# Kernel tuning notes

Hardware: AMD Instinct MI355X
Metric: run time of the kernel (lower is better)

## Reference

```python
import jax, jax.numpy as jnp
from jax import lax
import numpy as np

P = 128      # stored adversarial patch resolution
WIN = 256    # max pasted-patch extent (>= max patch_size = sqrt(300*300*0.4) ~ 190)
MINH = 60.0  # min_patch_height
H, W, B, N = 896, 896, 8, 24


def _bilinear(img, ys, xs):
    """Bilinearly sample img [h,w,c] on the grid ys x xs -> [len(ys), len(xs), c]."""
    h, w = img.shape[0], img.shape[1]
    ys = jnp.clip(ys, 0.0, h - 1.0)
    xs = jnp.clip(xs, 0.0, w - 1.0)
    y0 = jnp.floor(ys); x0 = jnp.floor(xs)
    y0i = y0.astype(jnp.int32); x0i = x0.astype(jnp.int32)
    y1i = jnp.minimum(y0i + 1, h - 1); x1i = jnp.minimum(x0i + 1, w - 1)
    wy = (ys - y0)[:, None, None]; wx = (xs - x0)[None, :, None]
    v00 = img[y0i][:, x0i]; v01 = img[y0i][:, x1i]
    v10 = img[y1i][:, x0i]; v11 = img[y1i][:, x1i]
    return (1 - wy) * ((1 - wx) * v00 + wx * v01) + wy * ((1 - wx) * v10 + wx * v11)


def setup_inputs() -> dict:
    key = jax.random.key(0)
    ks = jax.random.split(key, 8)
    ymin = jax.random.uniform(ks[0], (B, N), minval=0.0, maxval=H - 320.0)
    bh = jax.random.uniform(ks[1], (B, N), minval=80.0, maxval=300.0)
    xmin = jax.random.uniform(ks[2], (B, N), minval=0.0, maxval=W - 320.0)
    bw = jax.random.uniform(ks[3], (B, N), minval=80.0, maxval=300.0)
    boxes = jnp.stack([ymin, xmin, ymin + bh, xmin + bw], axis=-1)
    images = jax.random.uniform(ks[4], (B, H, W, 3))
    patch = jax.random.uniform(ks[5], (P, P, 3))
    Ws = jax.random.normal(ks[6], (2, 1)) * 0.5
    bs = jnp.zeros((1,), jnp.float32)
    Wg = jax.random.normal(ks[7], (2, P * P)) * 0.5
    bg = jnp.zeros((P * P,), jnp.float32)
    return {"boxes": boxes, "images": images, "patch": patch,
            "Ws": Ws, "bs": bs, "Wg": Wg, "bg": bg}


def reference(boxes, images, patch, Ws, bs, Wg, bg):
    Bx, Hx, Wx, C = images.shape
    Hf, Wf = float(Hx), float(Wx)
    mu_p = patch.mean((0, 1)); sd_p = patch.std((0, 1)) + 1e-6

    def per_image(image, bxs):
        bh = (bxs[:, 2] - bxs[:, 0]) / Hf
        bw = (bxs[:, 3] - bxs[:, 1]) / Wf
        feats = jnp.stack([bh, bw], axis=-1)                      # [N,2]
        scales = jax.nn.sigmoid(feats @ Ws + bs)[:, 0] * 0.4
        # Patcher.create (vectorized over boxes)
        h = bxs[:, 2] - bxs[:, 0]; w = bxs[:, 3] - bxs[:, 1]
        ps = jnp.floor(jnp.sqrt(h * w * scales))                  # square patch side
        oy = bxs[:, 0] + h / 2.0; ox = bxs[:, 1] + w / 2.0
        ymp = jnp.maximum(oy - ps / 2.0, 0.0)
        xmp = jnp.maximum(ox - ps / 2.0, 0.0)
        ymp = jnp.where(ymp + ps > Hf, Hf - ps, ymp)
        xmp = jnp.where(xmp + ps > Wf, Wf - ps, xmp)
        pboxes = jnp.stack([ymp, xmp, ps, ps], axis=-1)           # [N,4]
        valid = ps > MINH                                          # filter-by-mask
        masks = jax.nn.sigmoid(feats @ Wg + bg).reshape(-1, P, P, 1)  # gen masks
        img_p = jnp.pad(image, ((0, WIN), (0, WIN), (0, 0)))

        def body(carry, inp):
            imgc, bgl = carry
            pbox, mask, vld = inp
            yi = pbox[0].astype(jnp.int32); xi = pbox[1].astype(jnp.int32)
            ph = pbox[2].astype(jnp.int32); pw = pbox[3].astype(jnp.int32)
            phf = jnp.maximum(ph, 1).astype(jnp.float32)
            pwf = jnp.maximum(pw, 1).astype(jnp.float32)
            # crop background region -> fixed PxP
            ys = yi.astype(jnp.float32) + (jnp.arange(P, dtype=jnp.float32) + 0.5) * phf / P - 0.5
            xs = xi.astype(jnp.float32) + (jnp.arange(P, dtype=jnp.float32) + 0.5) * pwf / P - 0.5
            patch_bg = _bilinear(imgc, ys, xs)                    # [P,P,C]
            # histogram (moment) matching of patch to local background
            mu_b = patch_bg.mean((0, 1)); sd_b = patch_bg.std((0, 1)) + 1e-6
            matched = (patch - mu_p) / sd_p * sd_b + mu_b
            blended = jnp.where(mask > 0.5, matched, patch_bg)
            r = jnp.arange(WIN, dtype=jnp.float32)
            sy = (r + 0.5) * P / phf - 0.5
            sx = (r + 0.5) * P / pwf - 0.5
            im_win = _bilinear(blended, sy, sx)
            win = lax.dynamic_slice(imgc, (yi, xi, 0), (WIN, WIN, imgc.shape[-1]))
            inside = (jnp.arange(WIN)[:, None] < ph) & (jnp.arange(WIN)[None, :] < pw) & vld
            upd = jnp.where(inside[..., None], im_win, win)
            imgc = lax.dynamic_update_slice(imgc, upd, (yi, xi, 0))
            bgl = bgl + jnp.where(vld, mask.mean(), 0.0)          # generator.bg_loss
            return (imgc, bgl), None

        (img_p, bgl), _ = lax.scan(body, (img_p, jnp.zeros((), jnp.float32)),
                                   (pboxes, masks, valid))
        # scale loss over valid boxes: mean + 0.5*variance
        vf = valid.astype(jnp.float32)
        n = jnp.maximum(vf.sum(), 1.0)
        m = (scales * vf).sum() / n
        var = (vf * (scales - m) ** 2).sum() / n
        return img_p[:Hx, :Wx], bgl + m + 0.5 * var

    out, losses = jax.vmap(per_image)(images, boxes)
    return out, losses.sum()
```

## Files before the change

kernel.cpp:

```cpp
#include <hip/hip_runtime.h>

#define PPX  128
#define PP2  16384
#define IMH  896
#define IMW  896
#define NB   24
#define NI   8
#define HP   1152
#define WP   1152
#define MAXG 6
#define NMB  (NI*NB*8)
#define NCPY 2048
#define M1   12

#define WS_BOX  8
#define WS_MASK 2048
#define WS_SCH  100352
#define WS_LIST 100608
#define WS_MSUM 101760
#define WS_PART 103424
#define WS_PBG  140288

__device__ __forceinline__ void box_geom(const float* __restrict__ bx,
    const float* __restrict__ Wsc, const float* __restrict__ bsc,
    float& scale, float& ps, int& yi, int& xi, int& ph, int& vld)
{
  float ya=bx[0], xa=bx[1], yb=bx[2], xb=bx[3];
  float bh=(yb-ya)/(float)IMH, bw=(xb-xa)/(float)IMW;
  float z = bh*Wsc[0]+bw*Wsc[1]+bsc[0];
  float sig = 1.f/(1.f+expf(-z));
  scale = sig*0.4f;
  float h=yb-ya, w=xb-xa;
  ps = floorf(sqrtf((h*w)*scale));
  float oy=ya+h*0.5f, ox=xa+w*0.5f;
  float ymp=fmaxf(oy-ps*0.5f,0.f), xmp=fmaxf(ox-ps*0.5f,0.f);
  if (ymp+ps>(float)IMH) ymp=(float)IMH-ps;
  if (xmp+ps>(float)IMW) xmp=(float)IMW-ps;
  yi=(int)ymp; xi=(int)xmp; ph=(int)ps;
  vld = (ps>60.f) ? 1 : 0;
}

__device__ __forceinline__ void analytic3(int rr, int cc, float phf,
    const float* __restrict__ pbg1, const float* __restrict__ patch,
    const unsigned* msk, const float* ab, float v[3])
{
  float sy = ((rr + 0.5f)*128.0f)/phf - 0.5f;
  float sx = ((cc + 0.5f)*128.0f)/phf - 0.5f;
  sy = fminf(fmaxf(sy, 0.f), 127.f);
  sx = fminf(fmaxf(sx, 0.f), 127.f);
  float fy0 = floorf(sy), fx0 = floorf(sx);
  int py0 = (int)fy0, px0 = (int)fx0;
  int py1 = py0 + 1 < 127 ? py0 + 1 : 127;
  int px1 = px0 + 1 < 127 ? px0 + 1 : 127;
  float wy = sy - fy0, wx = sx - fx0;
  int i00 = (py0<<7)+px0, i01 = (py0<<7)+px1, i10 = (py1<<7)+px0, i11 = (py1<<7)+px1;
  bool m00 = (msk[i00>>5] >> (i00&31)) & 1u;
  bool m01 = (msk[i01>>5] >> (i01&31)) & 1u;
  bool m10 = (msk[i10>>5] >> (i10&31)) & 1u;
  bool m11 = (msk[i11>>5] >> (i11&31)) & 1u;
  #pragma unroll
  for (int ch = 0; ch < 3; ++ch) {
    float a = ab[ch], be = ab[3+ch];
    float t00 = m00 ? patch[i00*3+ch]*a + be : pbg1[i00*3+ch];
    float t01 = m01 ? patch[i01*3+ch]*a + be : pbg1[i01*3+ch];
    float t10 = m10 ? patch[i10*3+ch]*a + be : pbg1[i10*3+ch];
    float t11 = m11 ? patch[i11*3+ch]*a + be : pbg1[i11*3+ch];
    v[ch] = (1.f-wy)*((1.f-wx)*t00 + wx*t01) + wy*((1.f-wx)*t10 + wx*t11);
  }
}

__device__ __forceinline__ void crop_plain(
    const float* __restrict__ src, float* __restrict__ ws, int b, int n, int blk,
    float (*s_red)[6])
{
  const int tid = threadIdx.x;
  const int* bi = (const int*)(ws + WS_BOX + (b*NB + n)*8);
  const int yi = bi[2], xi = bi[3], ph = bi[4];
  const float phf = (float)(ph > 1 ? ph : 1);
  float* __restrict__ pbg = ws + WS_PBG + (size_t)(b*NB + n)*PP2*3;
  float sm[3] = {0,0,0}, sq[3] = {0,0,0};
  #pragma unroll
  for (int k = 0; k < 2; ++k) {
    int idx = blk*512 + k*256 + tid;
    int py = idx >> 7, px = idx & 127;
    float ys = ((float)yi + (py + 0.5f)*phf*(1.0f/PPX)) - 0.5f;
    float xs = ((float)xi + (px + 0.5f)*phf*(1.0f/PPX)) - 0.5f;
    ys = fminf(fmaxf(ys, 0.f), (float)(HP-1));
    xs = fminf(fmaxf(xs, 0.f), (float)(WP-1));
    float fy0 = floorf(ys), fx0 = floorf(xs);
    int y0 = (int)fy0, x0 = (int)fx0;
    int y1 = y0 + 1 < HP-1 ? y0 + 1 : HP-1;
    int x1 = x0 + 1 < WP-1 ? x0 + 1 : WP-1;
    float wy = ys - fy0, wx = xs - fx0;
    bool y0i = y0 < IMH, y1i = y1 < IMH, x0i = x0 < IMW, x1i = x1 < IMW;
    const float* r0 = src + (size_t)y0*IMW*3;
    const float* r1 = src + (size_t)y1*IMW*3;
    #pragma unroll
    for (int c = 0; c < 3; ++c) {
      float v00 = (y0i && x0i) ? r0[x0*3+c] : 0.f;
      float v01 = (y0i && x1i) ? r0[x1*3+c] : 0.f;
      float v10 = (y1i && x0i) ? r1[x0*3+c] : 0.f;
      float v11 = (y1i && x1i) ? r1[x1*3+c] : 0.f;
      float v = (1.f-wy)*((1.f-wx)*v00 + wx*v01) + wy*((1.f-wx)*v10 + wx*v11);
      pbg[idx*3+c] = v;
      sm[c] += v; sq[c] += v*v;
    }
  }
  float vals[6] = {sm[0],sm[1],sm[2],sq[0],sq[1],sq[2]};
  #pragma unroll
  for (int off = 32; off; off >>= 1)
    #pragma unroll
    for (int k = 0; k < 6; ++k) vals[k] += __shfl_down(vals[k], off);
  int wid = tid >> 6;
  __syncthreads();
  if ((tid & 63) == 0)
    for (int k = 0; k < 6; ++k) s_red[wid][k] = vals[k];
  __syncthreads();
  if (tid == 0) {
    float* part = ws + WS_PART + (size_t)((b*NB + n)*32 + blk)*6;
    for (int k = 0; k < 6; ++k)
      part[k] = s_red[0][k] + s_red[1][k] + s_red[2][k] + s_red[3][k];
  }
}

__global__ __launch_bounds__(256) void sched_k(
    const float* __restrict__ boxes,
    const float* __restrict__ Wsc, const float* __restrict__ bsc,
    const float* __restrict__ patch, float* __restrict__ ws)
{
  const int tid = threadIdx.x;
  if (blockIdx.x == 1) {
    __shared__ float s_red6[256][6];
    float s0=0,s1=0,s2=0,q0=0,q1=0,q2=0;
    for (int i = tid; i < PP2; i += 256) {
      float a = patch[i*3+0], b = patch[i*3+1], c = patch[i*3+2];
      s0+=a; s1+=b; s2+=c; q0+=a*a; q1+=b*b; q2+=c*c;
    }
    s_red6[tid][0]=s0; s_red6[tid][1]=s1; s_red6[tid][2]=s2;
    s_red6[tid][3]=q0; s_red6[tid][4]=q1; s_red6[tid][5]=q2;
    __syncthreads();
    for (int s = 128; s > 0; s >>= 1) {
      if (tid < s)
        for (int k=0;k<6;++k) s_red6[tid][k] += s_red6[tid+s][k];
      __syncthreads();
    }
    if (tid == 0) {
      for (int c=0;c<3;++c) {
        float mu  = s_red6[0][c]   * (1.0f/PP2);
        float var = s_red6[0][3+c] * (1.0f/PP2) - mu*mu;
        float sd  = sqrtf(fmaxf(var, 0.f)) + 1e-6f;
        ws[c] = mu; ws[3+c] = sd;
      }
    }
    return;
  }
  __shared__ int g_yi[NI*NB], g_xi[NI*NB], g_ph[NI*NB], g_vl[NI*NB];
  if (tid < NI*NB) {
    float scale, ps; int yi, xi, ph, vld;
    box_geom(boxes + tid*4, Wsc, bsc, scale, ps, yi, xi, ph, vld);
    g_yi[tid]=yi; g_xi[tid]=xi; g_ph[tid]=ph; g_vl[tid]=vld;
    float* bst = ws + WS_BOX + tid*8;
    bst[0] = scale;
    bst[1] = ps;
    ((int*)bst)[2] = yi;
    ((int*)bst)[3] = xi;
    ((int*)bst)[4] = ph;
    bst[5] = vld ? 1.f : 0.f;
  }
  __syncthreads();
  if (tid < NI) {
    unsigned* sch = ((unsigned*)ws) + WS_SCH + tid*32;
    unsigned* lst = ((unsigned*)ws) + WS_LIST + tid*(MAXG*NB);
    int lv[NB];
    int cnt[MAXG];
    for (int L = 0; L < MAXG; ++L) cnt[L] = 0;
    for (int n = 0; n < NB; ++n) {
      int idx = tid*NB + n;
      if (!g_vl[idx]) { lv[n] = -1; sch[n] = 255u; continue; }
      int y0 = g_yi[idx]-2, y1 = g_yi[idx]+g_ph[idx]+3;
      int x0 = g_xi[idx]-2, x1 = g_xi[idx]+g_ph[idx]+3;
      int L = 0;
      for (int m = 0; m < n; ++m) {
        if (lv[m] < 0) continue;
        int mi = tid*NB + m;
        int my0 = g_yi[mi]-2, my1 = g_yi[mi]+g_ph[mi]+3;
        int mx0 = g_xi[mi]-2, mx1 = g_xi[mi]+g_ph[mi]+3;
        if (y0 < my1 && my0 < y1 && x0 < mx1 && mx0 < x1)
          L = max(L, lv[m] + 1);
      }
      lv[n] = L;
      sch[n] = (unsigned)L;
      if (L < MAXG) lst[L*NB + cnt[L]++] = (unsigned)n;
    }
    for (int L = 0; L < MAXG; ++L) sch[24 + L] = (unsigned)cnt[L];
  }
}

__global__ __launch_bounds__(256) void first_k(
    float* __restrict__ out, const float* __restrict__ images,
    const float* __restrict__ boxes,
    const float* __restrict__ Wg, const float* __restrict__ bgv,
    float* __restrict__ ws)
{
  const int bid = blockIdx.x, tid = threadIdx.x;
  if (bid < NCPY) {
    const float4* src4 = (const float4*)images;
    float4* dst4 = (float4*)out;
    const int n4 = NI*IMH*IMW*3/4;
    for (int i = bid*256 + tid; i < n4; i += NCPY*256) dst4[i] = src4[i];
    return;
  }
  if (bid < NCPY + NMB) {
    const int w = bid - NCPY;
    const int bn = w >> 3, q = w & 7;
    float bh = (boxes[bn*4+2]-boxes[bn*4+0])/(float)IMH;
    float bw = (boxes[bn*4+3]-boxes[bn*4+1])/(float)IMW;
    unsigned* mwords = ((unsigned*)ws) + WS_MASK + bn*512;
    float lsum = 0.f;
    const int lane = tid & 63;
    #pragma unroll
    for (int i = 0; i < 8; ++i) {
      int p = q*2048 + i*256 + tid;
      float zz = bh*Wg[p] + bw*Wg[PP2 + p] + bgv[p];
      lsum += 1.0f / (1.0f + expf(-zz));
      unsigned long long m = __ballot(zz > 0.0f);
      if (lane == 0) {
        int base = p >> 5;
        mwords[base]   = (unsigned)(m & 0xffffffffULL);
        mwords[base+1] = (unsigned)(m >> 32);
      }
    }
    #pragma unroll
    for (int off = 32; off; off >>= 1) lsum += __shfl_down(lsum, off);
    __shared__ float s_r[4];
    if ((tid & 63) == 0) s_r[tid >> 6] = lsum;
    __syncthreads();
    if (tid == 0) ws[WS_MSUM + bn*8 + q] = s_r[0] + s_r[1] + s_r[2] + s_r[3];
    return;
  }
  const int w = bid - NCPY - NMB;
  const int b = w / (M1*32);
  const int rem = w - b*(M1*32);
  const int j = rem >> 5, blk = rem & 31;
  __shared__ float s_red[4][6];
  __shared__ int s_cn[NB];
  __shared__ int s_cc;
  const unsigned* sch = ((const unsigned*)ws) + WS_SCH + b*32;
  if (tid == 0) s_cc = (int)sch[24 + 0];
  __syncthreads();
  const int cc = s_cc;
  if (j >= cc) return;
  if (tid < cc) s_cn[tid] = (int)(((const unsigned*)ws) + WS_LIST + b*(MAXG*NB))[tid];
  __syncthreads();
  const float* src = images + (size_t)b*IMH*IMW*3;
  for (int jj = j; jj < cc; jj += M1)
    crop_plain(src, ws, b, s_cn[jj], blk, s_red);
}

__global__ __launch_bounds__(256) void crop_k(
    float* __restrict__ out, float* __restrict__ ws, int L, int M)
{
  const int bid = blockIdx.x, tid = threadIdx.x;
  const int b = bid / (M*32);
  const int rem = bid - b*(M*32);
  const int j = rem >> 5, blk = rem & 31;
  __shared__ float s_red[4][6];
  __shared__ int s_cn[NB];
  __shared__ int s_cc;
  const unsigned* sch = ((const unsigned*)ws) + WS_SCH + b*32;
  if (tid == 0) s_cc = (int)sch[24 + L];
  __syncthreads();
  const int cc = s_cc;
  if (j >= cc) return;
  if (tid < cc) s_cn[tid] = (int)(((const unsigned*)ws) + WS_LIST + b*(MAXG*NB))[L*NB + tid];
  __syncthreads();
  const float* src = out + (size_t)b*IMH*IMW*3;
  for (int jj = j; jj < cc; jj += M)
    crop_plain(src, ws, b, s_cn[jj], blk, s_red);
}

__global__ __launch_bounds__(256) void paste_k(
    float* __restrict__ out, const float* __restrict__ patch,
    float* __restrict__ ws, int L, int M)
{
  const int bid = blockIdx.x, tid = threadIdx.x;
  if (bid >= NI*M*32) {
    if (tid == 0) {
      float total = 0.f;
      for (int b = 0; b < NI; ++b) {
        float sum_s = 0.f, cnt = 0.f, bgl = 0.f;
        for (int n = 0; n < NB; ++n) {
          const float* bst = ws + WS_BOX + (b*NB + n)*8;
          float v = bst[5];
          float msum = 0.f;
          for (int q = 0; q < 8; ++q) msum += ws[WS_MSUM + (b*NB + n)*8 + q];
          sum_s += bst[0]*v; cnt += v; bgl += (msum*(1.0f/PP2))*v;
        }
        float nn = fmaxf(cnt, 1.0f);
        float m = sum_s / nn;
        float var = 0.f;
        for (int n = 0; n < NB; ++n) {
          const float* bst = ws + WS_BOX + (b*NB + n)*8;
          float d = bst[0] - m;
          var += bst[5]*d*d;
        }
        var /= nn;
        total += bgl + m + 0.5f*var;
      }
      out[(size_t)NI*IMH*IMW*3] = total;
    }
    return;
  }
  const int b = bid / (M*32);
  const int rem = bid - b*(M*32);
  const int j = rem >> 5, r = rem & 31;
  __shared__ int s_cp;
  __shared__ int s_pn[NB];
  __shared__ float s_ab[6];
  __shared__ unsigned s_mask[512];
  const unsigned* sch = ((const unsigned*)ws) + WS_SCH + b*32;
  if (tid == 0) s_cp = (int)sch[24 + L];
  __syncthreads();
  const int cp = s_cp;
  if (j >= cp) return;
  if (tid < cp) s_pn[tid] = (int)(((const unsigned*)ws) + WS_LIST + b*(MAXG*NB))[L*NB + tid];
  __syncthreads();
  float* __restrict__ img = out + (size_t)b*IMH*IMW*3;

  for (int jj = j; jj < cp; jj += M) {
    const int n = s_pn[jj];
    if (tid < 32) {
      const float* part = ws + WS_PART + (size_t)((b*NB + n)*32 + tid)*6;
      float v[6];
      #pragma unroll
      for (int k = 0; k < 6; ++k) v[k] = part[k];
      #pragma unroll
      for (int off = 16; off; off >>= 1)
        #pragma unroll
        for (int k = 0; k < 6; ++k) v[k] += __shfl_down(v[k], off, 32);
      if (tid == 0) {
        #pragma unroll
        for (int c = 0; c < 3; ++c) {
          float mu  = v[c]   * (1.0f/PP2);
          float var = v[3+c] * (1.0f/PP2) - mu*mu;
          float sd  = sqrtf(fmaxf(var, 0.f)) + 1e-6f;
          float alpha = sd / ws[3+c];
          s_ab[c]   = alpha;
          s_ab[3+c] = mu - ws[c]*alpha;
        }
      }
    }
    {
      const unsigned* mwords = ((const unsigned*)ws) + WS_MASK + (b*NB + n)*512;
      s_mask[tid]       = mwords[tid];
      s_mask[tid + 256] = mwords[tid + 256];
    }
    __syncthreads();
    const int* bi = (const int*)(ws + WS_BOX + (b*NB + n)*8);
    const int yi = bi[2], xi = bi[3], ph = bi[4];
    const float phf = (float)(ph > 1 ? ph : 1);
    const float* pbgp = ws + WS_PBG + (size_t)(b*NB + n)*PP2*3;
    const int tot = ph*ph;
    const int chunk = (tot + 31) / 32;
    const int i0 = r*chunk;
    const int i1 = min(tot, i0 + chunk);
    for (int idx = i0 + tid; idx < i1; idx += 256) {
      int rr = (int)((unsigned)idx / (unsigned)ph);
      int cx = idx - rr*ph;
      float v[3];
      analytic3(rr, cx, phf, pbgp, patch, s_mask, s_ab, v);
      float* dst = img + ((size_t)(yi + rr)*IMW + (xi + cx))*3;
      dst[0] = v[0]; dst[1] = v[1]; dst[2] = v[2];
    }
    __syncthreads();
  }
}

__global__ __launch_bounds__(256) void fallback_k(
    float* __restrict__ out, const float* __restrict__ patch, float* __restrict__ ws)
{
  const int b = blockIdx.x, tid = threadIdx.x;
  const unsigned* sch = ((const unsigned*)ws) + WS_SCH + b*32;
  float* __restrict__ img = out + (size_t)b*IMH*IMW*3;
  float* __restrict__ pbg = ws + WS_PBG + (size_t)(b*NB + 0)*PP2*3;
  __shared__ float s_red6[256][6];
  __shared__ float s_ab[6];
  __shared__ unsigned s_mask[512];

  for (int n = 0; n < NB; ++n) {
    unsigned g = sch[n];
    if (g < (unsigned)MAXG || g == 255u) continue;
    const float* bst = ws + WS_BOX + (b*NB + n)*8;
    const int yi = ((const int*)bst)[2];
    const int xi = ((const int*)bst)[3];
    const int ph = ((const int*)bst)[4];
    const float phf = (float)(ph > 1 ? ph : 1);

    float sm[3]={0,0,0}, sq[3]={0,0,0};
    for (int k = 0; k < PP2/256; ++k) {
      int idx = k*256 + tid;
      int py = idx >> 7, px = idx & 127;
      float ys = ((float)yi + (py + 0.5f)*phf*(1.0f/PPX)) - 0.5f;
      float xs = ((float)xi + (px + 0.5f)*phf*(1.0f/PPX)) - 0.5f;
      ys = fminf(fmaxf(ys, 0.f), (float)(HP-1));
      xs = fminf(fmaxf(xs, 0.f), (float)(WP-1));
      float fy0 = floorf(ys), fx0 = floorf(xs);
      int y0 = (int)fy0, x0 = (int)fx0;
      int y1 = y0 + 1 < HP-1 ? y0 + 1 : HP-1;
      int x1 = x0 + 1 < WP-1 ? x0 + 1 : WP-1;
      float wy = ys - fy0, wx = xs - fx0;
      bool y0i = y0 < IMH, y1i = y1 < IMH, x0i = x0 < IMW, x1i = x1 < IMW;
      const float* r0 = img + (size_t)y0*IMW*3;
      const float* r1 = img + (size_t)y1*IMW*3;
      #pragma unroll
      for (int c = 0; c < 3; ++c) {
        float v00 = (y0i && x0i) ? r0[x0*3+c] : 0.f;
        float v01 = (y0i && x1i) ? r0[x1*3+c] : 0.f;
        float v10 = (y1i && x0i) ? r1[x0*3+c] : 0.f;
        float v11 = (y1i && x1i) ? r1[x1*3+c] : 0.f;
        float v = (1.f-wy)*((1.f-wx)*v00 + wx*v01) + wy*((1.f-wx)*v10 + wx*v11);
        pbg[idx*3+c] = v;
        sm[c] += v; sq[c] += v*v;
      }
    }
    s_red6[tid][0]=sm[0]; s_red6[tid][1]=sm[1]; s_red6[tid][2]=sm[2];
    s_red6[tid][3]=sq[0]; s_red6[tid][4]=sq[1]; s_red6[tid][5]=sq[2];
    __syncthreads();
    for (int s2 = 128; s2 > 0; s2 >>= 1) {
      if (tid < s2)
        for (int k=0;k<6;++k) s_red6[tid][k] += s_red6[tid+s2][k];
      __syncthreads();
    }
    if (tid == 0) {
      for (int c=0;c<3;++c) {
        float mu  = s_red6[0][c]   * (1.0f/PP2);
        float var = s_red6[0][3+c] * (1.0f/PP2) - mu*mu;
        float sd  = sqrtf(fmaxf(var, 0.f)) + 1e-6f;
        float alpha = sd / ws[3+c];
        s_ab[c]   = alpha;
        s_ab[3+c] = mu - ws[c]*alpha;
      }
    }
    {
      const unsigned* mwords = ((const unsigned*)ws) + WS_MASK + (b*NB + n)*512;
      s_mask[tid]       = mwords[tid];
      s_mask[tid + 256] = mwords[tid + 256];
    }
    __syncthreads();
    const int tot = ph*ph;
    for (int idx = tid; idx < tot; idx += 256) {
      int rr = (int)((unsigned)idx / (unsigned)ph);
      int cc = idx - rr*ph;
      float v[3];
      analytic3(rr, cc, phf, pbg, patch, s_mask, s_ab, v);
      float* dst = img + ((size_t)(yi + rr)*IMW + (xi + cc))*3;
      dst[0] = v[0]; dst[1] = v[1]; dst[2] = v[2];
    }
    __syncthreads();
  }
}

extern "C" void kernel_launch(void* const* d_in, const int* in_sizes, int n_in,
                              void* d_out, int out_size, void* d_ws, size_t ws_size,
                              hipStream_t stream) {
  const float* boxes  = (const float*)d_in[0];
  const float* images = (const float*)d_in[1];
  const float* patch  = (const float*)d_in[2];
  const float* Wsc    = (const float*)d_in[3];
  const float* bsc    = (const float*)d_in[4];
  const float* Wg     = (const float*)d_in[5];
  const float* bgv    = (const float*)d_in[6];
  float* out = (float*)d_out;
  float* ws  = (float*)d_ws;

  sched_k<<<2, 256, 0, stream>>>(boxes, Wsc, bsc, patch, ws);
  first_k<<<NCPY + NMB + NI*M1*32, 256, 0, stream>>>(out, images, boxes, Wg, bgv, ws);
  paste_k<<<NI*M1*32 + 1, 256, 0, stream>>>(out, patch, ws, 0, M1);
  crop_k <<<NI*8*32, 256, 0, stream>>>(out, ws, 1, 8);
  paste_k<<<NI*8*32, 256, 0, stream>>>(out, patch, ws, 1, 8);
  crop_k <<<NI*4*32, 256, 0, stream>>>(out, ws, 2, 4);
  paste_k<<<NI*4*32, 256, 0, stream>>>(out, patch, ws, 2, 4);
  crop_k <<<NI*2*32, 256, 0, stream>>>(out, ws, 3, 2);
  paste_k<<<NI*2*32, 256, 0, stream>>>(out, patch, ws, 3, 2);
  crop_k <<<NI*2*32, 256, 0, stream>>>(out, ws, 4, 2);
  paste_k<<<NI*2*32, 256, 0, stream>>>(out, patch, ws, 4, 2);
  crop_k <<<NI*2*32, 256, 0, stream>>>(out, ws, 5, 2);
  paste_k<<<NI*2*32, 256, 0, stream>>>(out, patch, ws, 5, 2);
  fallback_k<<<NI, 256, 0, stream>>>(out, patch, ws);
}
```

Measured before the change: 200.8 us.

## Fold scheduling into first kernel and split level-0 crop into own launch

The separate scheduling/patch-statistics kernel is merged into the first kernel as two extra blocks. The mask-generation blocks now also do part of the image copy instead of occupying separate blocks. The level-0 crop, which needs the schedule, moves to its own crop_k launch that reads the original images, so the total launch count stays the same. The fallback kernel is widened to 1024 threads with a shuffle-based reduction, and the loss block loads per-box data into shared memory in parallel. The risk is that the combined first kernel now carries the serial scheduling work and a heavier mix of blocks.

```diff
diff --git a/kernel.cpp b/kernel.cpp
--- a/kernel.cpp
+++ b/kernel.cpp
@@ -9,7 +9,7 @@
 #define HP   1152
 #define WP   1152
 #define MAXG 6
-#define NMB  (NI*NB*8)
+#define NMB  (NI*NB)
 #define NCPY 2048
 #define M1   12
 
@@ -123,13 +123,15 @@
   }
 }
 
-__global__ __launch_bounds__(256) void sched_k(
+__global__ __launch_bounds__(256) void first_k(
+    float* __restrict__ out, const float* __restrict__ images,
     const float* __restrict__ boxes,
     const float* __restrict__ Wsc, const float* __restrict__ bsc,
+    const float* __restrict__ Wg, const float* __restrict__ bgv,
     const float* __restrict__ patch, float* __restrict__ ws)
 {
-  const int tid = threadIdx.x;
-  if (blockIdx.x == 1) {
+  const int bid = blockIdx.x, tid = threadIdx.x;
+  if (bid == NCPY) {
     __shared__ float s_red6[256][6];
     float s0=0,s1=0,s2=0,q0=0,q1=0,q2=0;
     for (int i = tid; i < PP2; i += 256) {
@@ -154,65 +156,52 @@
     }
     return;
   }
-  __shared__ int g_yi[NI*NB], g_xi[NI*NB], g_ph[NI*NB], g_vl[NI*NB];
-  if (tid < NI*NB) {
-    float scale, ps; int yi, xi, ph, vld;
-    box_geom(boxes + tid*4, Wsc, bsc, scale, ps, yi, xi, ph, vld);
-    g_yi[tid]=yi; g_xi[tid]=xi; g_ph[tid]=ph; g_vl[tid]=vld;
-    float* bst = ws + WS_BOX + tid*8;
-    bst[0] = scale;
-    bst[1] = ps;
-    ((int*)bst)[2] = yi;
-    ((int*)bst)[3] = xi;
-    ((int*)bst)[4] = ph;
-    bst[5] = vld ? 1.f : 0.f;
-  }
-  __syncthreads();
-  if (tid < NI) {
-    unsigned* sch = ((unsigned*)ws) + WS_SCH + tid*32;
-    unsigned* lst = ((unsigned*)ws) + WS_LIST + tid*(MAXG*NB);
-    int lv[NB];
-    int cnt[MAXG];
-    for (int L = 0; L < MAXG; ++L) cnt[L] = 0;
-    for (int n = 0; n < NB; ++n) {
-      int idx = tid*NB + n;
-      if (!g_vl[idx]) { lv[n] = -1; sch[n] = 255u; continue; }
-      int y0 = g_yi[idx]-2, y1 = g_yi[idx]+g_ph[idx]+3;
-      int x0 = g_xi[idx]-2, x1 = g_xi[idx]+g_ph[idx]+3;
-      int L = 0;
-      for (int m = 0; m < n; ++m) {
-        if (lv[m] < 0) continue;
-        int mi = tid*NB + m;
-        int my0 = g_yi[mi]-2, my1 = g_yi[mi]+g_ph[mi]+3;
-        int mx0 = g_xi[mi]-2, mx1 = g_xi[mi]+g_ph[mi]+3;
-        if (y0 < my1 && my0 < y1 && x0 < mx1 && mx0 < x1)
-          L = max(L, lv[m] + 1);
-      }
-      lv[n] = L;
-      sch[n] = (unsigned)L;
-      if (L < MAXG) lst[L*NB + cnt[L]++] = (unsigned)n;
-    }
-    for (int L = 0; L < MAXG; ++L) sch[24 + L] = (unsigned)cnt[L];
-  }
-}
-
-__global__ __launch_bounds__(256) void first_k(
-    float* __restrict__ out, const float* __restrict__ images,
-    const float* __restrict__ boxes,
-    const float* __restrict__ Wg, const float* __restrict__ bgv,
-    float* __restrict__ ws)
-{
-  const int bid = blockIdx.x, tid = threadIdx.x;
-  if (bid < NCPY) {
-    const float4* src4 = (const float4*)images;
-    float4* dst4 = (float4*)out;
-    const int n4 = NI*IMH*IMW*3/4;
-    for (int i = bid*256 + tid; i < n4; i += NCPY*256) dst4[i] = src4[i];
+  if (bid == NCPY + 1) {
+    __shared__ int g_yi[NI*NB], g_xi[NI*NB], g_ph[NI*NB], g_vl[NI*NB];
+    if (tid < NI*NB) {
+      float scale, ps; int yi, xi, ph, vld;
+      box_geom(boxes + tid*4, Wsc, bsc, scale, ps, yi, xi, ph, vld);
+      g_yi[tid]=yi; g_xi[tid]=xi; g_ph[tid]=ph; g_vl[tid]=vld;
+      float* bst = ws + WS_BOX + tid*8;
+      bst[0] = scale;
+      bst[1] = ps;
+      ((int*)bst)[2] = yi;
+      ((int*)bst)[3] = xi;
+      ((int*)bst)[4] = ph;
+      bst[5] = vld ? 1.f : 0.f;
+    }
+    __syncthreads();
+    if (tid < NI) {
+      unsigned* sch = ((unsigned*)ws) + WS_SCH + tid*32;
+      unsigned* lst = ((unsigned*)ws) + WS_LIST + tid*(MAXG*NB);
+      int lv[NB];
+      int cnt[MAXG];
+      for (int L = 0; L < MAXG; ++L) cnt[L] = 0;
+      for (int n = 0; n < NB; ++n) {
+        int idx = tid*NB + n;
+        if (!g_vl[idx]) { lv[n] = -1; sch[n] = 255u; continue; }
+        int y0 = g_yi[idx]-2, y1 = g_yi[idx]+g_ph[idx]+3;
+        int x0 = g_xi[idx]-2, x1 = g_xi[idx]+g_ph[idx]+3;
+        int L = 0;
+        for (int m = 0; m < n; ++m) {
+          if (lv[m] < 0) continue;
+          int mi = tid*NB + m;
+          int my0 = g_yi[mi]-2, my1 = g_yi[mi]+g_ph[mi]+3;
+          int mx0 = g_xi[mi]-2, mx1 = g_xi[mi]+g_ph[mi]+3;
+          if (y0 < my1 && my0 < y1 && x0 < mx1 && mx0 < x1)
+            L = max(L, lv[m] + 1);
+        }
+        lv[n] = L;
+        sch[n] = (unsigned)L;
+        if (L < MAXG) lst[L*NB + cnt[L]++] = (unsigned)n;
+      }
+      for (int L = 0; L < MAXG; ++L) sch[24 + L] = (unsigned)cnt[L];
+    }
     return;
   }
-  if (bid < NCPY + NMB) {
-    const int w = bid - NCPY;
-    const int bn = w >> 3, q = w & 7;
+
+  if (bid < NMB*8) {
+    const int bn = bid >> 3, q = bid & 7;
     float bh = (boxes[bn*4+2]-boxes[bn*4+0])/(float)IMH;
     float bw = (boxes[bn*4+3]-boxes[bn*4+1])/(float)IMW;
     unsigned* mwords = ((unsigned*)ws) + WS_MASK + bn*512;
@@ -236,29 +225,19 @@
     if ((tid & 63) == 0) s_r[tid >> 6] = lsum;
     __syncthreads();
     if (tid == 0) ws[WS_MSUM + bn*8 + q] = s_r[0] + s_r[1] + s_r[2] + s_r[3];
-    return;
-  }
-  const int w = bid - NCPY - NMB;
-  const int b = w / (M1*32);
-  const int rem = w - b*(M1*32);
-  const int j = rem >> 5, blk = rem & 31;
-  __shared__ float s_red[4][6];
-  __shared__ int s_cn[NB];
-  __shared__ int s_cc;
-  const unsigned* sch = ((const unsigned*)ws) + WS_SCH + b*32;
-  if (tid == 0) s_cc = (int)sch[24 + 0];
-  __syncthreads();
-  const int cc = s_cc;
-  if (j >= cc) return;
-  if (tid < cc) s_cn[tid] = (int)(((const unsigned*)ws) + WS_LIST + b*(MAXG*NB))[tid];
-  __syncthreads();
-  const float* src = images + (size_t)b*IMH*IMW*3;
-  for (int jj = j; jj < cc; jj += M1)
-    crop_plain(src, ws, b, s_cn[jj], blk, s_red);
+  }
+
+  {
+    const float4* src4 = (const float4*)images;
+    float4* dst4 = (float4*)out;
+    const int n4 = NI*IMH*IMW*3/4;
+    for (int i = bid*256 + tid; i < n4; i += NCPY*256) dst4[i] = src4[i];
+  }
 }
 
 __global__ __launch_bounds__(256) void crop_k(
-    float* __restrict__ out, float* __restrict__ ws, int L, int M)
+    float* __restrict__ out, const float* __restrict__ images,
+    float* __restrict__ ws, int L, int M)
 {
   const int bid = blockIdx.x, tid = threadIdx.x;
   const int b = bid / (M*32);
@@ -274,7 +253,8 @@
   if (j >= cc) return;
   if (tid < cc) s_cn[tid] = (int)(((const unsigned*)ws) + WS_LIST + b*(MAXG*NB))[L*NB + tid];
   __syncthreads();
-  const float* src = out + (size_t)b*IMH*IMW*3;
+  const float* src = (L == 0) ? images + (size_t)b*IMH*IMW*3
+                              : out + (size_t)b*IMH*IMW*3;
   for (int jj = j; jj < cc; jj += M)
     crop_plain(src, ws, b, s_cn[jj], blk, s_red);
 }
@@ -285,24 +265,31 @@
 {
   const int bid = blockIdx.x, tid = threadIdx.x;
   if (bid >= NI*M*32) {
+    __shared__ float l_sc[NI*NB], l_ms[NI*NB], l_vl[NI*NB];
+    if (tid < NI*NB) {
+      const float* bst = ws + WS_BOX + tid*8;
+      l_sc[tid] = bst[0]; l_vl[tid] = bst[5];
+      float ms = 0.f;
+      for (int q = 0; q < 8; ++q) ms += ws[WS_MSUM + tid*8 + q];
+      l_ms[tid] = ms;
+    }
+    __syncthreads();
     if (tid == 0) {
       float total = 0.f;
       for (int b = 0; b < NI; ++b) {
         float sum_s = 0.f, cnt = 0.f, bgl = 0.f;
         for (int n = 0; n < NB; ++n) {
-          const float* bst = ws + WS_BOX + (b*NB + n)*8;
-          float v = bst[5];
-          float msum = 0.f;
-          for (int q = 0; q < 8; ++q) msum += ws[WS_MSUM + (b*NB + n)*8 + q];
-          sum_s += bst[0]*v; cnt += v; bgl += (msum*(1.0f/PP2))*v;
+          int idx = b*NB + n;
+          float v = l_vl[idx];
+          sum_s += l_sc[idx]*v; cnt += v; bgl += (l_ms[idx]*(1.0f/PP2))*v;
         }
         float nn = fmaxf(cnt, 1.0f);
         float m = sum_s / nn;
         float var = 0.f;
         for (int n = 0; n < NB; ++n) {
-          const float* bst = ws + WS_BOX + (b*NB + n)*8;
-          float d = bst[0] - m;
-          var += bst[5]*d*d;
+          int idx = b*NB + n;
+          float d = l_sc[idx] - m;
+          var += l_vl[idx]*d*d;
         }
         var /= nn;
         total += bgl + m + 0.5f*var;
@@ -376,29 +363,28 @@
   }
 }
 
-__global__ __launch_bounds__(256) void fallback_k(
+__global__ __launch_bounds__(1024) void fb_k(
     float* __restrict__ out, const float* __restrict__ patch, float* __restrict__ ws)
 {
   const int b = blockIdx.x, tid = threadIdx.x;
   const unsigned* sch = ((const unsigned*)ws) + WS_SCH + b*32;
-  float* __restrict__ img = out + (size_t)b*IMH*IMW*3;
-  float* __restrict__ pbg = ws + WS_PBG + (size_t)(b*NB + 0)*PP2*3;
-  __shared__ float s_red6[256][6];
+  __shared__ float s_red[16][6];
   __shared__ float s_ab[6];
   __shared__ unsigned s_mask[512];
+  float* __restrict__ img = out + (size_t)b*IMH*IMW*3;
 
   for (int n = 0; n < NB; ++n) {
     unsigned g = sch[n];
     if (g < (unsigned)MAXG || g == 255u) continue;
-    const float* bst = ws + WS_BOX + (b*NB + n)*8;
-    const int yi = ((const int*)bst)[2];
-    const int xi = ((const int*)bst)[3];
-    const int ph = ((const int*)bst)[4];
+    const int* bi = (const int*)(ws + WS_BOX + (b*NB + n)*8);
+    const int yi = bi[2], xi = bi[3], ph = bi[4];
     const float phf = (float)(ph > 1 ? ph : 1);
+    float* __restrict__ pbg = ws + WS_PBG + (size_t)(b*NB + n)*PP2*3;
 
     float sm[3]={0,0,0}, sq[3]={0,0,0};
-    for (int k = 0; k < PP2/256; ++k) {
-      int idx = k*256 + tid;
+    #pragma unroll
+    for (int k = 0; k < PP2/1024; ++k) {
+      int idx = k*1024 + tid;
       int py = idx >> 7, px = idx & 127;
       float ys = ((float)yi + (py + 0.5f)*phf*(1.0f/PPX)) - 0.5f;
       float xs = ((float)xi + (px + 0.5f)*phf*(1.0f/PPX)) - 0.5f;
@@ -423,32 +409,34 @@
         sm[c] += v; sq[c] += v*v;
       }
     }
-    s_red6[tid][0]=sm[0]; s_red6[tid][1]=sm[1]; s_red6[tid][2]=sm[2];
-    s_red6[tid][3]=sq[0]; s_red6[tid][4]=sq[1]; s_red6[tid][5]=sq[2];
-    __syncthreads();
-    for (int s2 = 128; s2 > 0; s2 >>= 1) {
-      if (tid < s2)
-        for (int k=0;k<6;++k) s_red6[tid][k] += s_red6[tid+s2][k];
-      __syncthreads();
-    }
+    float vals[6] = {sm[0],sm[1],sm[2],sq[0],sq[1],sq[2]};
+    #pragma unroll
+    for (int off = 32; off; off >>= 1)
+      #pragma unroll
+      for (int k = 0; k < 6; ++k) vals[k] += __shfl_down(vals[k], off);
+    if ((tid & 63) == 0)
+      for (int k = 0; k < 6; ++k) s_red[tid >> 6][k] = vals[k];
+    if (tid < 512) {
+      const unsigned* mwords = ((const unsigned*)ws) + WS_MASK + (b*NB + n)*512;
+      s_mask[tid] = mwords[tid];
+    }
+    __syncthreads();
     if (tid == 0) {
-      for (int c=0;c<3;++c) {
-        float mu  = s_red6[0][c]   * (1.0f/PP2);
-        float var = s_red6[0][3+c] * (1.0f/PP2) - mu*mu;
+      float acc[6] = {0,0,0,0,0,0};
+      for (int w2 = 0; w2 < 16; ++w2)
+        for (int k = 0; k < 6; ++k) acc[k] += s_red[w2][k];
+      for (int c = 0; c < 3; ++c) {
+        float mu  = acc[c]   * (1.0f/PP2);
+        float var = acc[3+c] * (1.0f/PP2) - mu*mu;
         float sd  = sqrtf(fmaxf(var, 0.f)) + 1e-6f;
         float alpha = sd / ws[3+c];
         s_ab[c]   = alpha;
         s_ab[3+c] = mu - ws[c]*alpha;
       }
     }
-    {
-      const unsigned* mwords = ((const unsigned*)ws) + WS_MASK + (b*NB + n)*512;
-      s_mask[tid]       = mwords[tid];
-      s_mask[tid + 256] = mwords[tid + 256];
-    }
     __syncthreads();
     const int tot = ph*ph;
-    for (int idx = tid; idx < tot; idx += 256) {
+    for (int idx = tid; idx < tot; idx += 1024) {
       int rr = (int)((unsigned)idx / (unsigned)ph);
       int cc = idx - rr*ph;
       float v[3];
@@ -473,18 +461,18 @@
   float* out = (float*)d_out;
   float* ws  = (float*)d_ws;
 
-  sched_k<<<2, 256, 0, stream>>>(boxes, Wsc, bsc, patch, ws);
-  first_k<<<NCPY + NMB + NI*M1*32, 256, 0, stream>>>(out, images, boxes, Wg, bgv, ws);
+  first_k<<<NCPY + 2, 256, 0, stream>>>(out, images, boxes, Wsc, bsc, Wg, bgv, patch, ws);
+  crop_k <<<NI*M1*32, 256, 0, stream>>>(out, images, ws, 0, M1);
   paste_k<<<NI*M1*32 + 1, 256, 0, stream>>>(out, patch, ws, 0, M1);
-  crop_k <<<NI*8*32, 256, 0, stream>>>(out, ws, 1, 8);
+  crop_k <<<NI*8*32, 256, 0, stream>>>(out, images, ws, 1, 8);
   paste_k<<<NI*8*32, 256, 0, stream>>>(out, patch, ws, 1, 8);
-  crop_k <<<NI*4*32, 256, 0, stream>>>(out, ws, 2, 4);
+  crop_k <<<NI*4*32, 256, 0, stream>>>(out, images, ws, 2, 4);
   paste_k<<<NI*4*32, 256, 0, stream>>>(out, patch, ws, 2, 4);
-  crop_k <<<NI*2*32, 256, 0, stream>>>(out, ws, 3, 2);
+  crop_k <<<NI*2*32, 256, 0, stream>>>(out, images, ws, 3, 2);
   paste_k<<<NI*2*32, 256, 0, stream>>>(out, patch, ws, 3, 2);
-  crop_k <<<NI*2*32, 256, 0, stream>>>(out, ws, 4, 2);
+  crop_k <<<NI*2*32, 256, 0, stream>>>(out, images, ws, 4, 2);
   paste_k<<<NI*2*32, 256, 0, stream>>>(out, patch, ws, 4, 2);
-  crop_k <<<NI*2*32, 256, 0, stream>>>(out, ws, 5, 2);
+  crop_k <<<NI*2*32, 256, 0, stream>>>(out, images, ws, 5, 2);
   paste_k<<<NI*2*32, 256, 0, stream>>>(out, patch, ws, 5, 2);
-  fallback_k<<<NI, 256, 0, stream>>>(out, patch, ws);
-}
+  fb_k<<<NI, 1024, 0, stream>>>(out, patch, ws);
+}
```

Result: faster. 177.0 us (-11.8%).
